# Performance work log

Hardware: AMD Instinct MI355X
Metric: run time of the kernel (lower is better)

Reference implementation:

```python
import jax, jax.numpy as jnp
import numpy as np

B, T, H, D = 4, 4096, 16, 64
BLOCK_SIZE = 64      # BS: local block size
NUM_GLOBAL = 64      # G: global tokens (first G positions)
NUM_RANDOM = 192     # R: random key positions shared by all blocks


def setup_inputs() -> dict:
    key = jax.random.key(0)
    kq, kk, kv, kr = jax.random.split(key, 4)
    q = jax.random.normal(kq, (B, T, H, D), dtype=jnp.float32)
    k = jax.random.normal(kk, (B, T, H, D), dtype=jnp.float32)
    v = jax.random.normal(kv, (B, T, H, D), dtype=jnp.float32)
    # torch.randperm(src_len)[:R] -> no duplicate indices
    rand_idx = jax.random.permutation(kr, T)[:NUM_RANDOM].astype(jnp.int32)
    return {"q": q, "k": k, "v": v, "rand_idx": rand_idx}


def _bigbird(q, k, v, rand_idx):
    Bq, Tq, Hq, Dq = q.shape
    inv_scale = Dq ** (-0.5)
    G, BS, R = NUM_GLOBAL, BLOCK_SIZE, NUM_RANDOM

    # --- global queries: full attention over all keys ---
    gs = jnp.einsum('bghd,bkhd->bhgk', q[:, :G], k) * inv_scale
    gw = jax.nn.softmax(gs, axis=-1)
    out_g = jnp.einsum('bhgk,bkhd->bghd', gw, v)  # (B, G, H, D)

    # --- non-global queries: local block + global + random keys, one softmax ---
    nb = (Tq - G) // BS  # (T - G) divisible by BS by construction
    qb = q[:, G:].reshape(Bq, nb, BS, Hq, Dq)
    kb = k[:, G:].reshape(Bq, nb, BS, Hq, Dq)
    vb = v[:, G:].reshape(Bq, nb, BS, Hq, Dq)
    kg, vg = k[:, :G], v[:, :G]            # (B, G, H, D)
    kr, vr = k[:, rand_idx], v[:, rand_idx]  # (B, R, H, D)

    s_loc = jnp.einsum('bnlhd,bnkhd->bnhlk', qb, kb)   # (B, nb, H, BS, BS)
    s_glo = jnp.einsum('bnlhd,bkhd->bnhlk', qb, kg)    # (B, nb, H, BS, G)
    s_rnd = jnp.einsum('bnlhd,bkhd->bnhlk', qb, kr)    # (B, nb, H, BS, R)
    s = jnp.concatenate([s_loc, s_glo, s_rnd], axis=-1) * inv_scale
    w = jax.nn.softmax(s, axis=-1)  # joint softmax over local|global|random keys
    w_loc, w_glo, w_rnd = w[..., :BS], w[..., BS:BS + G], w[..., BS + G:]

    out_b = (jnp.einsum('bnhlk,bnkhd->bnlhd', w_loc, vb)
             + jnp.einsum('bnhlk,bkhd->bnlhd', w_glo, vg)
             + jnp.einsum('bnhlk,bkhd->bnlhd', w_rnd, vr))
    out_b = out_b.reshape(Bq, Tq - G, Hq, Dq)

    return jnp.concatenate([out_g, out_b], axis=1)  # (B, T, H, D)


def reference(q, k, v, rand_idx):
    return _bigbird(q, k, v, rand_idx)
```

## Files before the change

kernel.cpp:

```cpp
#include <hip/hip_runtime.h>
#include <math.h>
#include <stdint.h>

#define BB 4
#define TT 4096
#define HH 16
#define DD 64
#define GG 64
#define NRND 192
#define HD 1024
#define NBH 64
#define NCHUNK 8
#define NGBLK (NBH*NCHUNK)
#define NSPB  (NBH*63)

#define OFF_KBF  0u
#define OFF_VT   33554432u
#define OFF_VRT  67108864u
#define OFF_WACC 68681728u
#define OFF_WM   77070336u
#define OFF_WL   77201408u

typedef __attribute__((ext_vector_type(8))) short short8;
typedef __attribute__((ext_vector_type(16))) float f32x16;

__device__ __forceinline__ ushort rne_u(float f) {
    uint32_t u = __builtin_bit_cast(uint32_t, f);
    u += 0x7fffu + ((u >> 16) & 1u);
    return (ushort)(u >> 16);
}
__device__ __forceinline__ short bf_trunc_s(float f) {
    uint32_t u = __builtin_bit_cast(uint32_t, f);
    return (short)(u >> 16);
}
__device__ __forceinline__ float bf_back(short s) {
    uint32_t u = ((uint32_t)(uint16_t)s) << 16;
    return __builtin_bit_cast(float, u);
}

typedef const __attribute__((address_space(1))) uint32_t* gas1_t;
typedef __attribute__((address_space(3))) uint32_t* las3_t;
__device__ __forceinline__ void gld16(const void* g, void* l) {
    __builtin_amdgcn_global_load_lds((gas1_t)g, (las3_t)l, 16, 0, 0);
}

#define MEMFENCE asm volatile("" ::: "memory")

__global__ __launch_bounds__(256, 4)
void bb_prep(const float* __restrict__ K, const float* __restrict__ V,
             const int* __restrict__ RIDX, char* __restrict__ ws)
{
    __shared__ ushort vt_l[64][258];
    __shared__ int toks_c[NRND];
    const int bid = blockIdx.x, tid = threadIdx.x;

    if (bid < 8192) {
        const size_t gid = (size_t)bid * 256 + tid;
        const size_t r = gid >> 3;
        const int d0 = (int)(gid & 7) * 8;
        const float* src = K + r * 64 + d0;
        const float4 f0 = *(const float4*)src;
        const float4 f1 = *(const float4*)(src + 4);
        const int h = (int)(r & 15);
        const int t = (int)((r >> 4) & 4095);
        const int b = (int)(r >> 16);
        short8 o;
        o[0]=(short)rne_u(f0.x); o[1]=(short)rne_u(f0.y);
        o[2]=(short)rne_u(f0.z); o[3]=(short)rne_u(f0.w);
        o[4]=(short)rne_u(f1.x); o[5]=(short)rne_u(f1.y);
        o[6]=(short)rne_u(f1.z); o[7]=(short)rne_u(f1.w);
        ushort* dst = (ushort*)(ws + OFF_KBF) + (((size_t)(b*16 + h) * TT + t) * 64 + d0);
        *(short8*)dst = o;
    } else if (bid < 8192 + 1024) {
        const int id = bid - 8192;
        const int bh = id >> 4, tc = id & 15;
        const int b = bh >> 4, h = bh & 15;
        #pragma unroll
        for (int ch = 0; ch < 4; ++ch) {
            const int tl = ch * 64 + (tid >> 2);
            const int tok = tc * 256 + tl;
            const int d0 = (tid & 3) * 16;
            const float* src = V + ((size_t)(b * TT + tok) * HH + h) * DD + d0;
            #pragma unroll
            for (int i = 0; i < 16; i += 4) {
                const float4 f = *(const float4*)(src + i);
                vt_l[d0 + i    ][tl] = rne_u(f.x);
                vt_l[d0 + i + 1][tl] = rne_u(f.y);
                vt_l[d0 + i + 2][tl] = rne_u(f.z);
                vt_l[d0 + i + 3][tl] = rne_u(f.w);
            }
        }
        __syncthreads();
        const int d = tid >> 2, seg = tid & 3;
        #pragma unroll
        for (int j8 = 0; j8 < 8; ++j8) {
            const int bt = seg * 64 + j8 * 8;
            short8 o;
            #pragma unroll
            for (int e = 0; e < 8; ++e) o[e] = (short)vt_l[d][bt + e];
            char* dst = ws + OFF_VT + (size_t)bh * 524288 + (size_t)d * 8192 + (tc * 256 + bt) * 2;
            *(short8*)dst = o;
        }
    } else {
        const int bh = bid - 9216;
        const int b = bh >> 4, h = bh & 15;
        if (tid < NRND) toks_c[tid] = RIDX[tid];
        __syncthreads();
        #pragma unroll
        for (int ch = 0; ch < 3; ++ch) {
            const int slot = ch * 64 + (tid >> 2);
            const int tok = toks_c[slot];
            const int d0 = (tid & 3) * 16;
            const float* src = V + ((size_t)(b * TT + tok) * HH + h) * DD + d0;
            #pragma unroll
            for (int i = 0; i < 16; i += 4) {
                const float4 f = *(const float4*)(src + i);
                vt_l[d0 + i    ][slot] = rne_u(f.x);
                vt_l[d0 + i + 1][slot] = rne_u(f.y);
                vt_l[d0 + i + 2][slot] = rne_u(f.z);
                vt_l[d0 + i + 3][slot] = rne_u(f.w);
            }
        }
        __syncthreads();
        const int d = tid >> 2, seg = tid & 3;
        #pragma unroll
        for (int j = 0; j < 6; ++j) {
            const int s0 = seg * 48 + j * 8;
            short8 o;
            #pragma unroll
            for (int e = 0; e < 8; ++e) o[e] = (short)vt_l[d][s0 + e];
            char* dst = ws + OFF_VRT + (size_t)bh * 24576 + (size_t)d * 384 + s0 * 2;
            *(short8*)dst = o;
        }
    }
}

__global__ __launch_bounds__(256, 4)
void bb_mfma(const float* __restrict__ Q, const int* __restrict__ RIDX,
             float* __restrict__ OUT, char* __restrict__ ws)
{
    __shared__ __align__(16) char smem[32768];
    __shared__ float sm_m[2][64];
    __shared__ float sm_l[2][64];
    __shared__ int toks_s[NRND];
    float (*osum)[67] = (float(*)[67])smem;

    const int tid  = threadIdx.x;
    const int bid  = blockIdx.x;
    const int lane = tid & 63;
    const int wid  = tid >> 6;
    const int wq   = wid >> 1;
    const int wk   = wid & 1;
    const int lq   = lane & 31;
    const int lh   = lane >> 5;

    const bool is_glob = bid < NGBLK;
    int bh, qtok0, ntiles, kt0 = 0, chunk = 0;
    if (is_glob) {
        bh = bid >> 3; chunk = bid & 7; kt0 = chunk * 8;
        qtok0 = 0; ntiles = 8;
    } else {
        const int sid = bid - NGBLK;
        bh = sid & (NBH - 1);
        qtok0 = GG + (sid >> 6) * 64;
        ntiles = 5;
    }
    const int b  = bh >> 4;
    const int hd = bh & 15;
    const size_t bh_off = ((size_t)b * TT * HH + hd) * DD;

    const char* kbf_bh = ws + OFF_KBF + (size_t)bh * 524288;
    const char* vt_bh  = ws + OFF_VT  + (size_t)bh * 524288;
    const char* vrt_bh = ws + OFF_VRT + (size_t)bh * 24576;

    float4 qa[4], qb[4];
    {
        const float* qp = Q + bh_off + (size_t)(qtok0 + wq*32 + lq) * HD;
        #pragma unroll
        for (int ks = 0; ks < 4; ++ks) {
            qa[ks] = *(const float4*)(qp + ks*16 + lh*8);
            qb[ks] = *(const float4*)(qp + ks*16 + lh*8 + 4);
        }
    }
    if (!is_glob && tid < NRND) toks_s[tid] = RIDX[tid];

    auto stage_tile = [&](int buf, int kt_t) {
        const int rbase = wid * 16;
        #pragma unroll
        for (int i = 0; i < 2; ++i) {
            const int r0 = rbase + i*8;
            const int r  = r0 + (lane >> 3);
            const int cs = ((lane & 7) ^ (r & 7)) << 4;
            const char* ksrc;
            if (is_glob)           ksrc = kbf_bh + (size_t)((kt0 + kt_t)*64 + r)*128 + cs;
            else if (kt_t == 0)    ksrc = kbf_bh + (size_t)(qtok0 + r)*128 + cs;
            else if (kt_t == 1)    ksrc = kbf_bh + (size_t)r*128 + cs;
            else {
                const int tok = toks_s[(kt_t - 2)*64 + r];
                ksrc = kbf_bh + (size_t)tok*128 + cs;
            }
            gld16(ksrc, smem + buf*8192 + r0*128);
        }
        #pragma unroll
        for (int i = 0; i < 2; ++i) {
            const int r0 = rbase + i*8;
            const int d  = r0 + (lane >> 3);
            const int cs = ((lane & 7) ^ (d & 7)) << 4;
            const char* vsrc;
            if (is_glob)           vsrc = vt_bh + (size_t)d*8192 + (kt0 + kt_t)*128 + cs;
            else if (kt_t == 0)    vsrc = vt_bh + (size_t)d*8192 + qtok0*2 + cs;
            else if (kt_t == 1)    vsrc = vt_bh + (size_t)d*8192 + cs;
            else                   vsrc = vrt_bh + (size_t)d*384 + (kt_t - 2)*128 + cs;
            gld16(vsrc, smem + 16384 + buf*8192 + r0*128);
        }
    };

    stage_tile(0, 0);

    short8 qfh[4], qfl[4];
    #pragma unroll
    for (int ks = 0; ks < 4; ++ks) {
        float fv[8] = {qa[ks].x, qa[ks].y, qa[ks].z, qa[ks].w,
                       qb[ks].x, qb[ks].y, qb[ks].z, qb[ks].w};
        #pragma unroll
        for (int j = 0; j < 8; ++j) {
            const short hi = bf_trunc_s(fv[j]);
            qfh[ks][j] = hi;
            qfl[ks][j] = bf_trunc_s(fv[j] - bf_back(hi));
        }
    }

    f32x16 acc0, acc1;
    #pragma unroll
    for (int r = 0; r < 16; ++r) { acc0[r] = 0.f; acc1[r] = 0.f; }
    float m_run = -INFINITY, l_run = 0.f;

    for (int kt = 0; kt < ntiles; ++kt) {
        const int cur = kt & 1;
        const bool have_next = (kt + 1 < ntiles);
        if (have_next) stage_tile(cur ^ 1, kt + 1);
        MEMFENCE;
        if (have_next) asm volatile("s_waitcnt vmcnt(4) lgkmcnt(0)" ::: "memory");
        else           asm volatile("s_waitcnt vmcnt(0) lgkmcnt(0)" ::: "memory");
        __builtin_amdgcn_s_barrier();
        MEMFENCE;

        const char* kb = smem + cur*8192;
        const char* vb = smem + 16384 + cur*8192;

        f32x16 sc;
        #pragma unroll
        for (int r = 0; r < 16; ++r) sc[r] = 0.f;
        {
            const int krow = wk*32 + lq;
            const char* krp = kb + krow*128;
            const int ksw = (krow & 7) << 4;
            #pragma unroll
            for (int ks = 0; ks < 4; ++ks) {
                const short8 ak = *(const short8*)(krp + (((ks*2 + lh) << 4) ^ ksw));
                sc = __builtin_amdgcn_mfma_f32_32x32x16_bf16(ak, qfh[ks], sc, 0, 0, 0);
                sc = __builtin_amdgcn_mfma_f32_32x32x16_bf16(ak, qfl[ks], sc, 0, 0, 0);
            }
        }

        float pm = sc[0];
        #pragma unroll
        for (int r = 1; r < 16; ++r) pm = fmaxf(pm, sc[r]);
        pm *= 0.125f;
        pm = fmaxf(pm, __shfl_xor(pm, 32));
        const float mnew = fmaxf(m_run, pm);
        const float cf   = __expf(m_run - mnew);
        float p[16];
        float ls = 0.f;
        #pragma unroll
        for (int r = 0; r < 16; ++r) {
            p[r] = __expf(sc[r]*0.125f - mnew);
            ls += p[r];
        }
        ls += __shfl_xor(ls, 32);
        l_run = l_run * cf + ls;
        m_run = mnew;
        #pragma unroll
        for (int r = 0; r < 16; ++r) { acc0[r] *= cf; acc1[r] *= cf; }

        {
            const int vsw = (lq & 7) << 4;
            const char* v0p = vb + lq*128;
            const char* v1p = vb + (lq + 32)*128;
            #pragma unroll
            for (int s = 0; s < 2; ++s) {
                float sh[8];
                #pragma unroll
                for (int j = 0; j < 8; ++j) sh[j] = __shfl_xor(p[8*s + j], 32);
                short8 pf;
                #pragma unroll
                for (int j = 0; j < 8; ++j) {
                    float val;
                    if (lh == 0) val = (j < 4) ? p[8*s + j] : sh[j - 4];
                    else         val = (j < 4) ? sh[4 + j] : p[8*s + j];
                    uint32_t u = __builtin_bit_cast(uint32_t, val);
                    u += 0x7fffu + ((u >> 16) & 1u);
                    pf[j] = (short)(u >> 16);
                }
                const int cb = (wk*4 + s*2 + lh) << 4;
                const short8 a0 = *(const short8*)(v0p + (cb ^ vsw));
                const short8 a1 = *(const short8*)(v1p + (cb ^ vsw));
                acc0 = __builtin_amdgcn_mfma_f32_32x32x16_bf16(a0, pf, acc0, 0, 0, 0);
                acc1 = __builtin_amdgcn_mfma_f32_32x32x16_bf16(a1, pf, acc1, 0, 0, 0);
            }
        }
        MEMFENCE;
        __builtin_amdgcn_s_barrier();
        MEMFENCE;
    }

    if (lane < 32) { sm_m[wk][wq*32 + lq] = m_run; sm_l[wk][wq*32 + lq] = l_run; }
    __syncthreads();
    const int qrow = wq*32 + lq;
    const float Mq  = fmaxf(sm_m[0][qrow], sm_m[1][qrow]);
    const float wsc = __expf(m_run - Mq);
    if (wk == 0) {
        #pragma unroll
        for (int r = 0; r < 16; ++r) {
            const int dr = (r & 3) + 8*(r >> 2) + 4*lh;
            osum[qrow][dr     ] = acc0[r] * wsc;
            osum[qrow][dr + 32] = acc1[r] * wsc;
        }
    }
    __syncthreads();
    if (wk == 1) {
        #pragma unroll
        for (int r = 0; r < 16; ++r) {
            const int dr = (r & 3) + 8*(r >> 2) + 4*lh;
            osum[qrow][dr     ] += acc0[r] * wsc;
            osum[qrow][dr + 32] += acc1[r] * wsc;
        }
    }
    __syncthreads();
    {
        const int q  = tid >> 2;
        const int d0 = (tid & 3) * 16;
        const float M     = fmaxf(sm_m[0][q], sm_m[1][q]);
        const float lcomb = __expf(sm_m[0][q] - M) * sm_l[0][q]
                          + __expf(sm_m[1][q] - M) * sm_l[1][q];
        if (is_glob) {
            float* WACC = (float*)(ws + OFF_WACC);
            float* WM   = (float*)(ws + OFF_WM);
            float* WL   = (float*)(ws + OFF_WL);
            const int slot = chunk * NBH + bh;
            float* dst = WACC + (size_t)slot * 4096 + q * 64 + d0;
            #pragma unroll
            for (int i = 0; i < 16; i += 4) {
                float4 o;
                o.x = osum[q][d0 + i    ];
                o.y = osum[q][d0 + i + 1];
                o.z = osum[q][d0 + i + 2];
                o.w = osum[q][d0 + i + 3];
                *(float4*)(dst + i) = o;
            }
            if ((tid & 3) == 0) {
                WM[slot * 64 + q] = M;
                WL[slot * 64 + q] = lcomb;
            }
        } else {
            const float inv = 1.f / lcomb;
            float* dst = OUT + bh_off + (size_t)(qtok0 + q) * HD + d0;
            #pragma unroll
            for (int i = 0; i < 16; i += 4) {
                float4 o;
                o.x = osum[q][d0 + i    ] * inv;
                o.y = osum[q][d0 + i + 1] * inv;
                o.z = osum[q][d0 + i + 2] * inv;
                o.w = osum[q][d0 + i + 3] * inv;
                *(float4*)(dst + i) = o;
            }
        }
    }
}

__global__ __launch_bounds__(256, 4)
void bb_combine(const char* __restrict__ ws, float* __restrict__ OUT)
{
    const int bh = blockIdx.x;
    const int b  = bh >> 4;
    const int hd = bh & 15;
    const size_t bh_off = ((size_t)b * TT * HH + hd) * DD;

    const float* WACC = (const float*)(ws + OFF_WACC);
    const float* WM   = (const float*)(ws + OFF_WM);
    const float* WL   = (const float*)(ws + OFF_WL);

    const int q  = threadIdx.x >> 2;
    const int d0 = (threadIdx.x & 3) * 16;

    float m[NCHUNK];
    float M = -INFINITY;
    #pragma unroll
    for (int c = 0; c < NCHUNK; ++c) {
        m[c] = WM[(c * NBH + bh) * 64 + q];
        M = fmaxf(M, m[c]);
    }
    float w[NCHUNK];
    float denom = 0.f;
    #pragma unroll
    for (int c = 0; c < NCHUNK; ++c) {
        w[c] = __expf(m[c] - M);
        denom += w[c] * WL[(c * NBH + bh) * 64 + q];
    }
    const float inv = 1.f / denom;

    float* dst = OUT + bh_off + (size_t)q * HD + d0;
    #pragma unroll
    for (int i = 0; i < 16; i += 4) {
        float ox = 0.f, oy = 0.f, oz = 0.f, ow = 0.f;
        #pragma unroll
        for (int c = 0; c < NCHUNK; ++c) {
            const float4 a = *(const float4*)&WACC[(size_t)(c * NBH + bh) * 4096 + q * 64 + d0 + i];
            ox += w[c] * a.x; oy += w[c] * a.y;
            oz += w[c] * a.z; ow += w[c] * a.w;
        }
        float4 o; o.x = ox * inv; o.y = oy * inv; o.z = oz * inv; o.w = ow * inv;
        *(float4*)(dst + i) = o;
    }
}

extern "C" void kernel_launch(void* const* d_in, const int* in_sizes, int n_in,
                              void* d_out, int out_size, void* d_ws, size_t ws_size,
                              hipStream_t stream) {
    const float* Q    = (const float*)d_in[0];
    const float* K    = (const float*)d_in[1];
    const float* V    = (const float*)d_in[2];
    const int*   RIDX = (const int*)d_in[3];
    float* OUT = (float*)d_out;
    char*  ws  = (char*)d_ws;

    hipLaunchKernelGGL(bb_prep, dim3(8192 + 1024 + 64), dim3(256), 0, stream,
                       K, V, RIDX, ws);
    hipLaunchKernelGGL(bb_mfma, dim3(NGBLK + NSPB), dim3(256), 0, stream,
                       Q, RIDX, OUT, ws);
    hipLaunchKernelGGL(bb_combine, dim3(NBH), dim3(256), 0, stream, ws, OUT);
}
```

Measured before the change: 137.1 us.

## Single-buffer K/V tiles, chunk-major LDS layout, and remap blocks for occupancy

Shared memory drops from double-buffered 32 KB to a single 16 KB K/V buffer, and launch bounds rise to 8 blocks per CU so more waves can hide latency. The LDS layout becomes chunk-major (16-byte column chunks per row) in place of XOR swizzling, and the block-index mapping is permuted so neighbouring blocks cover different batch-heads. The cost is that loads are no longer overlapped with compute inside a block: each tile now needs a full wait and two barriers. The new layout may also cause LDS bank conflicts, and the higher occupancy target tightens register limits.

```diff
diff --git a/kernel.cpp b/kernel.cpp
--- a/kernel.cpp
+++ b/kernel.cpp
@@ -135,18 +135,19 @@
     }
 }
 
-__global__ __launch_bounds__(256, 4)
+__global__ __launch_bounds__(256, 8)
 void bb_mfma(const float* __restrict__ Q, const int* __restrict__ RIDX,
              float* __restrict__ OUT, char* __restrict__ ws)
 {
-    __shared__ __align__(16) char smem[32768];
+    __shared__ __align__(16) char smem[17408];
     __shared__ float sm_m[2][64];
     __shared__ float sm_l[2][64];
     __shared__ int toks_s[NRND];
+    char* kbuf = smem;
+    char* vbuf = smem + 8192;
     float (*osum)[67] = (float(*)[67])smem;
 
     const int tid  = threadIdx.x;
-    const int bid  = blockIdx.x;
     const int lane = tid & 63;
     const int wid  = tid >> 6;
     const int wq   = wid >> 1;
@@ -154,15 +155,20 @@
     const int lq   = lane & 31;
     const int lh   = lane >> 5;
 
-    const bool is_glob = bid < NGBLK;
+    const int j = blockIdx.x;
+    const bool is_glob = j < NGBLK;
     int bh, qtok0, ntiles, kt0 = 0, chunk = 0;
     if (is_glob) {
-        bh = bid >> 3; chunk = bid & 7; kt0 = chunk * 8;
+        const int jj = j >> 3;
+        bh    = (j & 7) + 8 * (jj & 7);
+        chunk = jj >> 3;
+        kt0   = chunk * 8;
         qtok0 = 0; ntiles = 8;
     } else {
-        const int sid = bid - NGBLK;
-        bh = sid & (NBH - 1);
-        qtok0 = GG + (sid >> 6) * 64;
+        const int js = j - NGBLK;
+        const int jj = js >> 3;
+        bh    = (js & 7) + 8 * (jj & 7);
+        qtok0 = GG + (jj >> 3) * 64;
         ntiles = 5;
     }
     const int b  = bh >> 4;
@@ -184,38 +190,33 @@
     }
     if (!is_glob && tid < NRND) toks_s[tid] = RIDX[tid];
 
-    auto stage_tile = [&](int buf, int kt_t) {
-        const int rbase = wid * 16;
+    auto stage_tile = [&](int kt_t) {
         #pragma unroll
         for (int i = 0; i < 2; ++i) {
-            const int r0 = rbase + i*8;
-            const int r  = r0 + (lane >> 3);
-            const int cs = ((lane & 7) ^ (r & 7)) << 4;
+            const int c = wid*2 + i;
             const char* ksrc;
-            if (is_glob)           ksrc = kbf_bh + (size_t)((kt0 + kt_t)*64 + r)*128 + cs;
-            else if (kt_t == 0)    ksrc = kbf_bh + (size_t)(qtok0 + r)*128 + cs;
-            else if (kt_t == 1)    ksrc = kbf_bh + (size_t)r*128 + cs;
+            if (is_glob)        ksrc = kbf_bh + (size_t)((kt0 + kt_t)*64 + lane)*128 + c*16;
+            else if (kt_t == 0) ksrc = kbf_bh + (size_t)(qtok0 + lane)*128 + c*16;
+            else if (kt_t == 1) ksrc = kbf_bh + (size_t)lane*128 + c*16;
             else {
-                const int tok = toks_s[(kt_t - 2)*64 + r];
-                ksrc = kbf_bh + (size_t)tok*128 + cs;
-            }
-            gld16(ksrc, smem + buf*8192 + r0*128);
+                const int tok = toks_s[(kt_t - 2)*64 + lane];
+                ksrc = kbf_bh + (size_t)tok*128 + c*16;
+            }
+            gld16(ksrc, kbuf + c*1024);
         }
         #pragma unroll
         for (int i = 0; i < 2; ++i) {
-            const int r0 = rbase + i*8;
-            const int d  = r0 + (lane >> 3);
-            const int cs = ((lane & 7) ^ (d & 7)) << 4;
+            const int c = wid*2 + i;
             const char* vsrc;
-            if (is_glob)           vsrc = vt_bh + (size_t)d*8192 + (kt0 + kt_t)*128 + cs;
-            else if (kt_t == 0)    vsrc = vt_bh + (size_t)d*8192 + qtok0*2 + cs;
-            else if (kt_t == 1)    vsrc = vt_bh + (size_t)d*8192 + cs;
-            else                   vsrc = vrt_bh + (size_t)d*384 + (kt_t - 2)*128 + cs;
-            gld16(vsrc, smem + 16384 + buf*8192 + r0*128);
+            if (is_glob)        vsrc = vt_bh + (size_t)lane*8192 + ((kt0 + kt_t)*64 + c*8)*2;
+            else if (kt_t == 0) vsrc = vt_bh + (size_t)lane*8192 + (qtok0 + c*8)*2;
+            else if (kt_t == 1) vsrc = vt_bh + (size_t)lane*8192 + c*16;
+            else                vsrc = vrt_bh + (size_t)lane*384 + ((kt_t - 2)*64 + c*8)*2;
+            gld16(vsrc, vbuf + c*1024);
         }
     };
 
-    stage_tile(0, 0);
+    stage_tile(0);
 
     short8 qfh[4], qfl[4];
     #pragma unroll
@@ -223,10 +224,10 @@
         float fv[8] = {qa[ks].x, qa[ks].y, qa[ks].z, qa[ks].w,
                        qb[ks].x, qb[ks].y, qb[ks].z, qb[ks].w};
         #pragma unroll
-        for (int j = 0; j < 8; ++j) {
-            const short hi = bf_trunc_s(fv[j]);
-            qfh[ks][j] = hi;
-            qfl[ks][j] = bf_trunc_s(fv[j] - bf_back(hi));
+        for (int jj = 0; jj < 8; ++jj) {
+            const short hi = bf_trunc_s(fv[jj]);
+            qfh[ks][jj] = hi;
+            qfl[ks][jj] = bf_trunc_s(fv[jj] - bf_back(hi));
         }
     }
 
@@ -235,29 +236,20 @@
     for (int r = 0; r < 16; ++r) { acc0[r] = 0.f; acc1[r] = 0.f; }
     float m_run = -INFINITY, l_run = 0.f;
 
+    MEMFENCE;
+    asm volatile("s_waitcnt vmcnt(0) lgkmcnt(0)" ::: "memory");
+    __builtin_amdgcn_s_barrier();
+    MEMFENCE;
+
     for (int kt = 0; kt < ntiles; ++kt) {
-        const int cur = kt & 1;
-        const bool have_next = (kt + 1 < ntiles);
-        if (have_next) stage_tile(cur ^ 1, kt + 1);
-        MEMFENCE;
-        if (have_next) asm volatile("s_waitcnt vmcnt(4) lgkmcnt(0)" ::: "memory");
-        else           asm volatile("s_waitcnt vmcnt(0) lgkmcnt(0)" ::: "memory");
-        __builtin_amdgcn_s_barrier();
-        MEMFENCE;
-
-        const char* kb = smem + cur*8192;
-        const char* vb = smem + 16384 + cur*8192;
-
         f32x16 sc;
         #pragma unroll
         for (int r = 0; r < 16; ++r) sc[r] = 0.f;
         {
             const int krow = wk*32 + lq;
-            const char* krp = kb + krow*128;
-            const int ksw = (krow & 7) << 4;
             #pragma unroll
             for (int ks = 0; ks < 4; ++ks) {
-                const short8 ak = *(const short8*)(krp + (((ks*2 + lh) << 4) ^ ksw));
+                const short8 ak = *(const short8*)(kbuf + (ks*2 + lh)*1024 + krow*16);
                 sc = __builtin_amdgcn_mfma_f32_32x32x16_bf16(ak, qfh[ks], sc, 0, 0, 0);
                 sc = __builtin_amdgcn_mfma_f32_32x32x16_bf16(ak, qfl[ks], sc, 0, 0, 0);
             }
@@ -283,35 +275,38 @@
         #pragma unroll
         for (int r = 0; r < 16; ++r) { acc0[r] *= cf; acc1[r] *= cf; }
 
-        {
-            const int vsw = (lq & 7) << 4;
-            const char* v0p = vb + lq*128;
-            const char* v1p = vb + (lq + 32)*128;
-            #pragma unroll
-            for (int s = 0; s < 2; ++s) {
-                float sh[8];
-                #pragma unroll
-                for (int j = 0; j < 8; ++j) sh[j] = __shfl_xor(p[8*s + j], 32);
-                short8 pf;
-                #pragma unroll
-                for (int j = 0; j < 8; ++j) {
-                    float val;
-                    if (lh == 0) val = (j < 4) ? p[8*s + j] : sh[j - 4];
-                    else         val = (j < 4) ? sh[4 + j] : p[8*s + j];
-                    uint32_t u = __builtin_bit_cast(uint32_t, val);
-                    u += 0x7fffu + ((u >> 16) & 1u);
-                    pf[j] = (short)(u >> 16);
-                }
-                const int cb = (wk*4 + s*2 + lh) << 4;
-                const short8 a0 = *(const short8*)(v0p + (cb ^ vsw));
-                const short8 a1 = *(const short8*)(v1p + (cb ^ vsw));
-                acc0 = __builtin_amdgcn_mfma_f32_32x32x16_bf16(a0, pf, acc0, 0, 0, 0);
-                acc1 = __builtin_amdgcn_mfma_f32_32x32x16_bf16(a1, pf, acc1, 0, 0, 0);
-            }
-        }
-        MEMFENCE;
-        __builtin_amdgcn_s_barrier();
-        MEMFENCE;
+        #pragma unroll
+        for (int s = 0; s < 2; ++s) {
+            float sh[8];
+            #pragma unroll
+            for (int jj = 0; jj < 8; ++jj) sh[jj] = __shfl_xor(p[8*s + jj], 32);
+            short8 pf;
+            #pragma unroll
+            for (int jj = 0; jj < 8; ++jj) {
+                float val;
+                if (lh == 0) val = (jj < 4) ? p[8*s + jj] : sh[jj - 4];
+                else         val = (jj < 4) ? sh[4 + jj] : p[8*s + jj];
+                uint32_t u = __builtin_bit_cast(uint32_t, val);
+                u += 0x7fffu + ((u >> 16) & 1u);
+                pf[jj] = (short)(u >> 16);
+            }
+            const int cb = wk*4 + s*2 + lh;
+            const short8 a0 = *(const short8*)(vbuf + cb*1024 + lq*16);
+            const short8 a1 = *(const short8*)(vbuf + cb*1024 + (lq + 32)*16);
+            acc0 = __builtin_amdgcn_mfma_f32_32x32x16_bf16(a0, pf, acc0, 0, 0, 0);
+            acc1 = __builtin_amdgcn_mfma_f32_32x32x16_bf16(a1, pf, acc1, 0, 0, 0);
+        }
+
+        if (kt + 1 < ntiles) {
+            MEMFENCE;
+            __builtin_amdgcn_s_barrier();
+            MEMFENCE;
+            stage_tile(kt + 1);
+            MEMFENCE;
+            asm volatile("s_waitcnt vmcnt(0)" ::: "memory");
+            __builtin_amdgcn_s_barrier();
+            MEMFENCE;
+        }
     }
 
     if (lane < 32) { sm_m[wk][wq*32 + lq] = m_run; sm_l[wk][wq*32 + lq] = l_run; }
```

After: 322.7 us. 2.35x slower.
